# Performance work log

Measured on AMD Instinct MI355X. Metric: run time of the kernel, lower is better.

Reference implementation:

```python
import jax, jax.numpy as jnp
import numpy as np

B, T, C = 8, 1024, 1024   # batch, seq (== block_size), n_embed
H, D = 16, 64             # num_heads, head_size


def setup_inputs() -> dict:
    key = jax.random.key(0)
    kx, kq, kk, kv = jax.random.split(key, 4)
    scale = C ** -0.5  # mimic nn.Linear init scale roughly
    return {
        "x": jax.random.normal(kx, (B, T, C), dtype=jnp.float32),
        "Wq": jax.random.normal(kq, (H, C, D), dtype=jnp.float32) * scale,
        "Wk": jax.random.normal(kk, (H, C, D), dtype=jnp.float32) * scale,
        "Wv": jax.random.normal(kv, (H, C, D), dtype=jnp.float32) * scale,
    }


def reference(x, Wq, Wk, Wv):
    # Per-head Q/K/V projections (batched over heads instead of a Python loop)
    q = jnp.einsum("btc,hcd->bhtd", x, Wq)
    k = jnp.einsum("btc,hcd->bhtd", x, Wk)
    v = jnp.einsum("btc,hcd->bhtd", x, Wv)

    # scaled causal attention scores: [B, H, T, T]
    scores = jnp.einsum("bhtd,bhsd->bhts", q, k) * (D ** -0.5)
    causal = jnp.tril(jnp.ones((T, T), dtype=bool))
    scores = jnp.where(causal, scores, jnp.finfo(scores.dtype).min)
    attn = jax.nn.softmax(scores, axis=-1)

    out = jnp.einsum("bhts,bhsd->bhtd", attn, v)  # [B, H, T, D]
    # concat heads along last dim -> [B, T, H*D]
    return out.transpose(0, 2, 1, 3).reshape(B, T, H * D)
```

## Files before the change

### kernel.cpp

```cpp
#include <hip/hip_runtime.h>
#include <hip/hip_bf16.h>
#include <cstdint>


typedef __attribute__((ext_vector_type(8))) short short8;
typedef __attribute__((ext_vector_type(4))) short bfs4;
typedef __attribute__((ext_vector_type(4))) float f32x4;
typedef __attribute__((ext_vector_type(4))) int   i32x4;

__device__ __forceinline__ unsigned short f2bf(float f) {
  union { float f; unsigned int u; } v; v.f = f;
  unsigned int u = v.u;
  return (unsigned short)((u + 0x7fffu + ((u >> 16) & 1u)) >> 16);
}

__device__ __forceinline__ unsigned int pk_bf16(float a, float b) {
  union { __hip_bfloat162 h; unsigned int u; } cv;
  cv.h = __float22bfloat162_rn(make_float2(a, b));
  return cv.u;
}

__global__ __launch_bounds__(256) void k_convert_x(const float* __restrict__ x,
                                                   unsigned short* __restrict__ xb) {
  int g = blockIdx.x * 256 + threadIdx.x;
  const float4* xp = (const float4*)x + (size_t)g * 2;
  float4 a = xp[0], b = xp[1];
  short8 o;
  o[0] = (short)f2bf(a.x); o[1] = (short)f2bf(a.y);
  o[2] = (short)f2bf(a.z); o[3] = (short)f2bf(a.w);
  o[4] = (short)f2bf(b.x); o[5] = (short)f2bf(b.y);
  o[6] = (short)f2bf(b.z); o[7] = (short)f2bf(b.w);
  *(short8*)(xb + (size_t)g * 8) = o;
}

__global__ __launch_bounds__(256) void k_convert_w(const float* __restrict__ Wq,
                                                   const float* __restrict__ Wk,
                                                   const float* __restrict__ Wv,
                                                   unsigned short* __restrict__ Wt) {
  int g = blockIdx.x * 256 + threadIdx.x;
  int d  = g & 63;
  int cb = (g >> 6) & 127;
  int h  = (g >> 13) & 15;
  int p  = g >> 17;
  const float* W = (p == 0) ? Wq : (p == 1) ? Wk : Wv;
  const float* src = W + ((size_t)h * 1024 + cb * 8) * 64 + d;
  short8 o;
#pragma unroll
  for (int j = 0; j < 8; ++j) o[j] = (short)f2bf(src[(size_t)j * 64]);
  *(short8*)(Wt + (((size_t)p * 16 + h) * 64 + d) * 1024 + cb * 8) = o;
}

__global__ __launch_bounds__(256) void k_proj(const unsigned short* __restrict__ xb,
                                              const unsigned short* __restrict__ Wt,
                                              unsigned short* __restrict__ Qb,
                                              unsigned short* __restrict__ Kb,
                                              unsigned short* __restrict__ Vt) {
  __shared__ alignas(16) unsigned short As[8192];
  __shared__ alignas(16) unsigned short Bs[8192];
  const int p   = blockIdx.y;
  const int bx  = blockIdx.x;
  const int tid = threadIdx.x;
  const int lane = tid & 63, w = tid >> 6;
  const int ln = lane & 15, quad = lane >> 4;
  const int wm = w >> 1, wn = w & 1;

  const unsigned short* Abase;
  const unsigned short* Bbase;
  int m0, n0;
  const int c = bx & 7, j = bx >> 3;
  if (p < 2) {
    Abase = xb; Bbase = Wt + (size_t)p * 1048576;
    m0 = ((j >> 3) * 8 + c) * 128;
    n0 = (j & 7) * 128;
  } else {
    Abase = Wt + (size_t)2 * 1048576; Bbase = xb;
    n0 = ((j >> 3) * 8 + c) * 128;
    m0 = (j & 7) * 128;
  }

  i32x4 ra[4], rb[4];
  auto ld = [&](int kt) {
    const int c0 = kt * 64;
#pragma unroll
    for (int i = 0; i < 4; ++i) {
      int idx = i * 256 + tid;
      int iln = idx & 15, iq = (idx >> 4) & 3, imt = (idx >> 6) & 7, ikk = (idx >> 9) & 1;
      int row = imt * 16 + iln;
      int col = c0 + ikk * 32 + iq * 8;
      ra[i] = *(const i32x4*)(Abase + (size_t)(m0 + row) * 1024 + col);
      rb[i] = *(const i32x4*)(Bbase + (size_t)(n0 + row) * 1024 + col);
    }
  };

  f32x4 acc[4][4];
#pragma unroll
  for (int i = 0; i < 4; ++i)
#pragma unroll
    for (int jj = 0; jj < 4; ++jj) acc[i][jj] = (f32x4){0.f, 0.f, 0.f, 0.f};

  ld(0);
  for (int kt = 0; kt < 16; ++kt) {
#pragma unroll
    for (int i = 0; i < 4; ++i) {
      *(i32x4*)((char*)As + (size_t)(i * 256 + tid) * 16) = ra[i];
      *(i32x4*)((char*)Bs + (size_t)(i * 256 + tid) * 16) = rb[i];
    }
    __syncthreads();
    if (kt < 15) ld(kt + 1);

#pragma unroll
    for (int kk = 0; kk < 2; ++kk) {
      short8 af[4], bfr[4];
#pragma unroll
      for (int t4 = 0; t4 < 4; ++t4) {
        af[t4]  = *(const short8*)&As[(size_t)((((kk * 8 + wm * 4 + t4) * 4 + quad) * 16 + ln)) * 8];
        bfr[t4] = *(const short8*)&Bs[(size_t)((((kk * 8 + wn * 4 + t4) * 4 + quad) * 16 + ln)) * 8];
      }
#pragma unroll
      for (int mt = 0; mt < 4; ++mt)
#pragma unroll
        for (int nt = 0; nt < 4; ++nt)
          acc[mt][nt] = __builtin_amdgcn_mfma_f32_16x16x32_bf16(
              af[mt], bfr[nt], acc[mt][nt], 0, 0, 0);
    }
    __syncthreads();
  }

  unsigned short* outp = (p == 0) ? Qb : (p == 1) ? Kb : Vt;
#pragma unroll
  for (int mt = 0; mt < 4; ++mt)
#pragma unroll
    for (int nt = 0; nt < 4; ++nt)
#pragma unroll
      for (int r = 0; r < 4; ++r) {
        int m = m0 + (wm * 4 + mt) * 16 + quad * 4 + r;
        int n = n0 + (wn * 4 + nt) * 16 + ln;
        size_t addr;
        if (p < 2) {
          addr = ((size_t)(m >> 10) * 16 + (n >> 6)) * 65536 + (size_t)(m & 1023) * 64 + (n & 63);
        } else {
          addr = ((size_t)(n >> 10) * 1024 + m) * 1024 + (n & 1023);
        }
        outp[addr] = f2bf(acc[mt][nt][r]);
      }
}

__global__ __launch_bounds__(256) void k_attn(const unsigned short* __restrict__ Qb,
                                              const unsigned short* __restrict__ Kb,
                                              const unsigned short* __restrict__ Vt,
                                              float* __restrict__ out) {
  __shared__ alignas(16) unsigned short Ks[4096];
  __shared__ alignas(16) unsigned short Vs[4096];
  __shared__ alignas(16) unsigned short Ps[8192];
  const int bid = blockIdx.x;
  const int qb = 7 - (bid >> 7);
  const int bh = bid & 127;
  const int b = bh >> 4, h = bh & 15;
  const int tid = threadIdx.x, lane = tid & 63, w = tid >> 6;
  const int ln = lane & 15, quad = lane >> 4;

  i32x4 rk[2], rv[2];
  auto ldkv = [&](int kt) {
    const int s0 = kt * 64;
#pragma unroll
    for (int i = 0; i < 2; ++i) {
      int idx = i * 256 + tid;
      int iln = idx & 15, iq = (idx >> 4) & 3, ikk = (idx >> 6) & 1, it = (idx >> 7) & 3;
      rk[i] = *(const i32x4*)(Kb + ((size_t)bh * 1024 + s0 + it * 16 + iln) * 64 + ikk * 32 + iq * 8);
      rv[i] = *(const i32x4*)(Vt + ((size_t)bh * 64 + it * 16 + iln) * 1024 + s0 + ikk * 32 + iq * 8);
    }
  };

  short8 qf[2][2];
#pragma unroll
  for (int qt = 0; qt < 2; ++qt) {
    const int q = qb * 128 + qt * 64 + w * 16 + ln;
#pragma unroll
    for (int kk = 0; kk < 2; ++kk)
      qf[qt][kk] = *(const short8*)(Qb + ((size_t)bh * 1024 + q) * 64 + kk * 32 + quad * 8);
  }

  f32x4 o[2][4];
#pragma unroll
  for (int qt = 0; qt < 2; ++qt)
#pragma unroll
    for (int dt = 0; dt < 4; ++dt) o[qt][dt] = (f32x4){0.f, 0.f, 0.f, 0.f};
  float l_i[2] = {0.f, 0.f};
  const float sc = 0.18033688011112042f;
  const float FM = 16.0f;

  const int ktmax = 2 * qb + 1;
  ldkv(0);

  for (int kt = 0; kt <= ktmax; ++kt) {
    const int s0 = kt * 64;
#pragma unroll
    for (int i = 0; i < 2; ++i) {
      *(i32x4*)((char*)Ks + (size_t)(i * 256 + tid) * 16) = rk[i];
      *(i32x4*)((char*)Vs + (size_t)(i * 256 + tid) * 16) = rv[i];
    }
    __syncthreads();
    if (kt < ktmax) ldkv(kt + 1);

    f32x4 st[2][4];
#pragma unroll
    for (int s = 0; s < 4; ++s) {
      st[0][s] = (f32x4){0.f, 0.f, 0.f, 0.f};
      st[1][s] = (f32x4){0.f, 0.f, 0.f, 0.f};
#pragma unroll
      for (int kk = 0; kk < 2; ++kk) {
        short8 kf = *(const short8*)&Ks[(size_t)(((s * 2 + kk) * 4 + quad) * 16 + ln) * 8];
        st[0][s] = __builtin_amdgcn_mfma_f32_16x16x32_bf16(kf, qf[0][kk], st[0][s], 0, 0, 0);
        st[1][s] = __builtin_amdgcn_mfma_f32_16x16x32_bf16(kf, qf[1][kk], st[1][s], 0, 0, 0);
      }
    }

#pragma unroll
    for (int qt = 0; qt < 2; ++qt) {
      const int q = qb * 128 + qt * 64 + w * 16 + ln;
      const bool masked = (kt >= 2 * qb + qt);
      float pv[4][4];
      float rs = 0.f;
#pragma unroll
      for (int s = 0; s < 4; ++s)
#pragma unroll
        for (int r = 0; r < 4; ++r) {
          float v = fmaf(st[qt][s][r], sc, -FM);
          if (masked) {
            int sidx = s0 + s * 16 + quad * 4 + r;
            if (sidx > q) v = -1.0e30f;
          }
          float e = __builtin_amdgcn_exp2f(v);
          pv[s][r] = e;
          rs += e;
        }
      rs += __shfl_xor(rs, 16);
      rs += __shfl_xor(rs, 32);
      l_i[qt] += rs;

      unsigned short* Pq = Ps + (w * 2 + qt) * 1024;
#pragma unroll
      for (int s = 0; s < 4; ++s) {
        union { bfs4 v; unsigned int u[2]; } pk;
        pk.u[0] = pk_bf16(pv[s][0], pv[s][1]);
        pk.u[1] = pk_bf16(pv[s][2], pv[s][3]);
        *(bfs4*)&Pq[(s * 2 + (quad >> 1)) * 128 + ln * 8 + (quad & 1) * 4] = pk.v;
      }
    }

#pragma unroll
    for (int kk = 0; kk < 2; ++kk) {
      short8 pf0 = *(const short8*)&Ps[(size_t)(w * 2 + 0) * 1024 + (size_t)((kk * 4 + quad) * 16 + ln) * 8];
      short8 pf1 = *(const short8*)&Ps[(size_t)(w * 2 + 1) * 1024 + (size_t)((kk * 4 + quad) * 16 + ln) * 8];
#pragma unroll
      for (int dt = 0; dt < 4; ++dt) {
        short8 vf = *(const short8*)&Vs[(size_t)(((dt * 2 + kk) * 4 + quad) * 16 + ln) * 8];
        o[0][dt] = __builtin_amdgcn_mfma_f32_16x16x32_bf16(vf, pf0, o[0][dt], 0, 0, 0);
        o[1][dt] = __builtin_amdgcn_mfma_f32_16x16x32_bf16(vf, pf1, o[1][dt], 0, 0, 0);
      }
    }

    __syncthreads();
  }

#pragma unroll
  for (int qt = 0; qt < 2; ++qt) {
    const int q = qb * 128 + qt * 64 + w * 16 + ln;
    const float rl = 1.0f / l_i[qt];
#pragma unroll
    for (int dt = 0; dt < 4; ++dt) {
      float4 ov;
      ov.x = o[qt][dt][0] * rl; ov.y = o[qt][dt][1] * rl;
      ov.z = o[qt][dt][2] * rl; ov.w = o[qt][dt][3] * rl;
      *(float4*)(out + ((size_t)b * 1024 + q) * 1024 + h * 64 + dt * 16 + quad * 4) = ov;
    }
  }
}

extern "C" void kernel_launch(void* const* d_in, const int* in_sizes, int n_in,
                              void* d_out, int out_size, void* d_ws, size_t ws_size,
                              hipStream_t stream) {
  const float* x  = (const float*)d_in[0];
  const float* Wq = (const float*)d_in[1];
  const float* Wk = (const float*)d_in[2];
  const float* Wv = (const float*)d_in[3];
  float* out = (float*)d_out;

  unsigned short* ws = (unsigned short*)d_ws;
  unsigned short* xb = ws;
  unsigned short* Wt = ws + 8388608;
  unsigned short* Qb = ws + 11534336;
  unsigned short* Kb = ws + 19922944;
  unsigned short* Vt = ws + 28311552;

  hipLaunchKernelGGL(k_convert_x, dim3(4096), dim3(256), 0, stream, x, xb);
  hipLaunchKernelGGL(k_convert_w, dim3(1536), dim3(256), 0, stream, Wq, Wk, Wv, Wt);
  hipLaunchKernelGGL(k_proj, dim3(512, 3), dim3(256), 0, stream, xb, Wt, Qb, Kb, Vt);
  hipLaunchKernelGGL(k_attn, dim3(1024), dim3(256), 0, stream, Qb, Kb, Vt, out);
}
```

Baseline: 232.0 us.

## Load GEMM and attention tiles directly into LDS via global_load_lds

Replaces the register-staged prefetch (global load to VGPRs, then LDS store) in both the projection GEMM and the attention kernel with direct global-to-LDS 16-byte loads. This cuts VGPR pressure and the LDS write instructions. It also drops the software prefetch of the next tile, so each iteration now waits on its own load before computing, and global latency is no longer overlapped with the MFMA work. No waitcnt is added beyond __syncthreads, so correctness relies on the compiler inserting vmcnt waits.

```diff
diff --git a/kernel.cpp b/kernel.cpp
--- a/kernel.cpp
+++ b/kernel.cpp
@@ -6,7 +6,6 @@
 typedef __attribute__((ext_vector_type(8))) short short8;
 typedef __attribute__((ext_vector_type(4))) short bfs4;
 typedef __attribute__((ext_vector_type(4))) float f32x4;
-typedef __attribute__((ext_vector_type(4))) int   i32x4;
 
 __device__ __forceinline__ unsigned short f2bf(float f) {
   union { float f; unsigned int u; } v; v.f = f;
@@ -18,6 +17,12 @@
   union { __hip_bfloat162 h; unsigned int u; } cv;
   cv.h = __float22bfloat162_rn(make_float2(a, b));
   return cv.u;
+}
+
+__device__ __forceinline__ void gload_lds16(const void* g, void* l) {
+  __builtin_amdgcn_global_load_lds(
+      (const __attribute__((address_space(1))) void*)g,
+      (__attribute__((address_space(3))) void*)l, 16, 0, 0);
 }
 
 __global__ __launch_bounds__(256) void k_convert_x(const float* __restrict__ x,
@@ -78,8 +83,7 @@
     m0 = (j & 7) * 128;
   }
 
-  i32x4 ra[4], rb[4];
-  auto ld = [&](int kt) {
+  auto stage = [&](int kt) {
     const int c0 = kt * 64;
 #pragma unroll
     for (int i = 0; i < 4; ++i) {
@@ -87,8 +91,9 @@
       int iln = idx & 15, iq = (idx >> 4) & 3, imt = (idx >> 6) & 7, ikk = (idx >> 9) & 1;
       int row = imt * 16 + iln;
       int col = c0 + ikk * 32 + iq * 8;
-      ra[i] = *(const i32x4*)(Abase + (size_t)(m0 + row) * 1024 + col);
-      rb[i] = *(const i32x4*)(Bbase + (size_t)(n0 + row) * 1024 + col);
+      const int chunk0 = i * 256 + (tid & 192);
+      gload_lds16(Abase + (size_t)(m0 + row) * 1024 + col, (char*)As + (size_t)chunk0 * 16);
+      gload_lds16(Bbase + (size_t)(n0 + row) * 1024 + col, (char*)Bs + (size_t)chunk0 * 16);
     }
   };
 
@@ -98,15 +103,9 @@
 #pragma unroll
     for (int jj = 0; jj < 4; ++jj) acc[i][jj] = (f32x4){0.f, 0.f, 0.f, 0.f};
 
-  ld(0);
   for (int kt = 0; kt < 16; ++kt) {
-#pragma unroll
-    for (int i = 0; i < 4; ++i) {
-      *(i32x4*)((char*)As + (size_t)(i * 256 + tid) * 16) = ra[i];
-      *(i32x4*)((char*)Bs + (size_t)(i * 256 + tid) * 16) = rb[i];
-    }
-    __syncthreads();
-    if (kt < 15) ld(kt + 1);
+    stage(kt);
+    __syncthreads();
 
 #pragma unroll
     for (int kk = 0; kk < 2; ++kk) {
@@ -159,18 +158,6 @@
   const int tid = threadIdx.x, lane = tid & 63, w = tid >> 6;
   const int ln = lane & 15, quad = lane >> 4;
 
-  i32x4 rk[2], rv[2];
-  auto ldkv = [&](int kt) {
-    const int s0 = kt * 64;
-#pragma unroll
-    for (int i = 0; i < 2; ++i) {
-      int idx = i * 256 + tid;
-      int iln = idx & 15, iq = (idx >> 4) & 3, ikk = (idx >> 6) & 1, it = (idx >> 7) & 3;
-      rk[i] = *(const i32x4*)(Kb + ((size_t)bh * 1024 + s0 + it * 16 + iln) * 64 + ikk * 32 + iq * 8);
-      rv[i] = *(const i32x4*)(Vt + ((size_t)bh * 64 + it * 16 + iln) * 1024 + s0 + ikk * 32 + iq * 8);
-    }
-  };
-
   short8 qf[2][2];
 #pragma unroll
   for (int qt = 0; qt < 2; ++qt) {
@@ -190,17 +177,20 @@
   const float FM = 16.0f;
 
   const int ktmax = 2 * qb + 1;
-  ldkv(0);
 
   for (int kt = 0; kt <= ktmax; ++kt) {
     const int s0 = kt * 64;
 #pragma unroll
     for (int i = 0; i < 2; ++i) {
-      *(i32x4*)((char*)Ks + (size_t)(i * 256 + tid) * 16) = rk[i];
-      *(i32x4*)((char*)Vs + (size_t)(i * 256 + tid) * 16) = rv[i];
-    }
-    __syncthreads();
-    if (kt < ktmax) ldkv(kt + 1);
+      int idx = i * 256 + tid;
+      int iln = idx & 15, iq = (idx >> 4) & 3, ikk = (idx >> 6) & 1, it = (idx >> 7) & 3;
+      const int chunk0 = i * 256 + (tid & 192);
+      gload_lds16(Kb + ((size_t)bh * 1024 + s0 + it * 16 + iln) * 64 + ikk * 32 + iq * 8,
+                  (char*)Ks + (size_t)chunk0 * 16);
+      gload_lds16(Vt + ((size_t)bh * 64 + it * 16 + iln) * 1024 + s0 + ikk * 32 + iq * 8,
+                  (char*)Vs + (size_t)chunk0 * 16);
+    }
+    __syncthreads();
 
     f32x4 st[2][4];
 #pragma unroll
```

New measurement: 237.4 us. +2.3%, slower.

## Rewrite projection GEMM with 256x256 tiles and double-buffered direct-to-LDS loads

Applied to the files above, without the earlier changes.

The QKV projection GEMM moves from 128x128 tiles with 256 threads to 256x256 tiles with 512 threads (8 waves), which raises operand reuse per block. Global loads now go straight into double-buffered LDS via global_load_lds, so the register staging round-trip disappears. Loads for the next k-step are interleaved with the MFMA phases using barriers and setprio. In exchange, 384 large blocks at one block per CU may underfill the GPU and leave a tail, and LDS use is much higher.

```diff
diff --git a/kernel.cpp b/kernel.cpp
--- a/kernel.cpp
+++ b/kernel.cpp
@@ -18,6 +18,12 @@
   union { __hip_bfloat162 h; unsigned int u; } cv;
   cv.h = __float22bfloat162_rn(make_float2(a, b));
   return cv.u;
+}
+
+__device__ __forceinline__ void gload_lds16(const void* g, void* l) {
+  __builtin_amdgcn_global_load_lds(
+      (const __attribute__((address_space(1))) void*)g,
+      (__attribute__((address_space(3))) void*)l, 16, 0, 0);
 }
 
 __global__ __launch_bounds__(256) void k_convert_x(const float* __restrict__ x,
@@ -50,91 +56,133 @@
   *(short8*)(Wt + (((size_t)p * 16 + h) * 64 + d) * 1024 + cb * 8) = o;
 }
 
-__global__ __launch_bounds__(256) void k_proj(const unsigned short* __restrict__ xb,
-                                              const unsigned short* __restrict__ Wt,
-                                              unsigned short* __restrict__ Qb,
-                                              unsigned short* __restrict__ Kb,
-                                              unsigned short* __restrict__ Vt) {
-  __shared__ alignas(16) unsigned short As[8192];
-  __shared__ alignas(16) unsigned short Bs[8192];
+__global__ __launch_bounds__(512, 1) void k_proj(const unsigned short* __restrict__ xb,
+                                                 const unsigned short* __restrict__ Wt,
+                                                 unsigned short* __restrict__ Qb,
+                                                 unsigned short* __restrict__ Kb,
+                                                 unsigned short* __restrict__ Vt) {
+  __shared__ alignas(16) unsigned short As[2][2][8192];
+  __shared__ alignas(16) unsigned short Bs[2][2][8192];
   const int p   = blockIdx.y;
   const int bx  = blockIdx.x;
   const int tid = threadIdx.x;
   const int lane = tid & 63, w = tid >> 6;
   const int ln = lane & 15, quad = lane >> 4;
-  const int wm = w >> 1, wn = w & 1;
+  const int wm = w >> 2, wn = w & 3;
 
   const unsigned short* Abase;
   const unsigned short* Bbase;
   int m0, n0;
-  const int c = bx & 7, j = bx >> 3;
   if (p < 2) {
     Abase = xb; Bbase = Wt + (size_t)p * 1048576;
-    m0 = ((j >> 3) * 8 + c) * 128;
-    n0 = (j & 7) * 128;
+    m0 = (bx >> 2) * 256;
+    n0 = (bx & 3) * 256;
   } else {
     Abase = Wt + (size_t)2 * 1048576; Bbase = xb;
-    n0 = ((j >> 3) * 8 + c) * 128;
-    m0 = (j & 7) * 128;
-  }
-
-  i32x4 ra[4], rb[4];
-  auto ld = [&](int kt) {
-    const int c0 = kt * 64;
-#pragma unroll
-    for (int i = 0; i < 4; ++i) {
-      int idx = i * 256 + tid;
-      int iln = idx & 15, iq = (idx >> 4) & 3, imt = (idx >> 6) & 7, ikk = (idx >> 9) & 1;
-      int row = imt * 16 + iln;
-      int col = c0 + ikk * 32 + iq * 8;
-      ra[i] = *(const i32x4*)(Abase + (size_t)(m0 + row) * 1024 + col);
-      rb[i] = *(const i32x4*)(Bbase + (size_t)(n0 + row) * 1024 + col);
+    m0 = (bx & 3) * 256;
+    n0 = (bx >> 2) * 256;
+  }
+
+  auto stageA = [&](int buf, int half, int t) {
+#pragma unroll
+    for (int i = 0; i < 2; ++i) {
+      int c = i * 512 + tid;
+      int iln = c & 15, iq = (c >> 4) & 3, lm = (c >> 6) & 7, ikk = (c >> 9) & 1;
+      int row = m0 + half * 128 + lm * 16 + iln;
+      int col = t * 64 + ikk * 32 + iq * 8;
+      const int chunk0 = i * 512 + w * 64;
+      gload_lds16(Abase + (size_t)row * 1024 + col,
+                  (char*)&As[buf][half][0] + (size_t)chunk0 * 16);
     }
   };
-
-  f32x4 acc[4][4];
-#pragma unroll
-  for (int i = 0; i < 4; ++i)
+  auto stageB = [&](int buf, int half, int t) {
+#pragma unroll
+    for (int i = 0; i < 2; ++i) {
+      int c = i * 512 + tid;
+      int iln = c & 15, iq = (c >> 4) & 3, lm = (c >> 6) & 7, ikk = (c >> 9) & 1;
+      int row = n0 + half * 128 + lm * 16 + iln;
+      int col = t * 64 + ikk * 32 + iq * 8;
+      const int chunk0 = i * 512 + w * 64;
+      gload_lds16(Bbase + (size_t)row * 1024 + col,
+                  (char*)&Bs[buf][half][0] + (size_t)chunk0 * 16);
+    }
+  };
+
+  f32x4 acc[8][4];
+#pragma unroll
+  for (int i = 0; i < 8; ++i)
 #pragma unroll
     for (int jj = 0; jj < 4; ++jj) acc[i][jj] = (f32x4){0.f, 0.f, 0.f, 0.f};
 
-  ld(0);
-  for (int kt = 0; kt < 16; ++kt) {
-#pragma unroll
-    for (int i = 0; i < 4; ++i) {
-      *(i32x4*)((char*)As + (size_t)(i * 256 + tid) * 16) = ra[i];
-      *(i32x4*)((char*)Bs + (size_t)(i * 256 + tid) * 16) = rb[i];
-    }
-    __syncthreads();
-    if (kt < 15) ld(kt + 1);
-
-#pragma unroll
-    for (int kk = 0; kk < 2; ++kk) {
-      short8 af[4], bfr[4];
-#pragma unroll
-      for (int t4 = 0; t4 < 4; ++t4) {
-        af[t4]  = *(const short8*)&As[(size_t)((((kk * 8 + wm * 4 + t4) * 4 + quad) * 16 + ln)) * 8];
-        bfr[t4] = *(const short8*)&Bs[(size_t)((((kk * 8 + wn * 4 + t4) * 4 + quad) * 16 + ln)) * 8];
-      }
-#pragma unroll
-      for (int mt = 0; mt < 4; ++mt)
-#pragma unroll
-        for (int nt = 0; nt < 4; ++nt)
-          acc[mt][nt] = __builtin_amdgcn_mfma_f32_16x16x32_bf16(
-              af[mt], bfr[nt], acc[mt][nt], 0, 0, 0);
-    }
-    __syncthreads();
+  stageA(0, 0, 0); stageA(0, 1, 0); stageB(0, 0, 0); stageB(0, 1, 0);
+  asm volatile("s_waitcnt vmcnt(0)" ::: "memory");
+  __builtin_amdgcn_s_barrier();
+
+  for (int it = 0; it < 8; ++it) {
+    const int t1 = 2 * it + 1;
+    const int t2 = 2 * it + 2;
+    const bool st2 = (t2 < 16);
+#pragma unroll
+    for (int ph = 0; ph < 8; ++ph) {
+      const int rbuf = ph >> 2;
+      const int q = ph & 3;
+      const int mh = q >> 1, nq = q & 1;
+
+      const unsigned short* Ah = As[rbuf][wm];
+      const unsigned short* Bh = Bs[rbuf][wn >> 1];
+      short8 af[4][2], bf[2][2];
+#pragma unroll
+      for (int m = 0; m < 4; ++m)
+#pragma unroll
+        for (int kk = 0; kk < 2; ++kk)
+          af[m][kk] = *(const short8*)&Ah[(size_t)(kk * 512 + (mh * 4 + m) * 64 + quad * 16 + ln) * 8];
+#pragma unroll
+      for (int n = 0; n < 2; ++n)
+#pragma unroll
+        for (int kk = 0; kk < 2; ++kk)
+          bf[n][kk] = *(const short8*)&Bh[(size_t)(kk * 512 + ((wn & 1) * 4 + nq * 2 + n) * 64 + quad * 16 + ln) * 8];
+
+      if (rbuf == 0) {
+        if      (q == 0) stageA(1, 0, t1);
+        else if (q == 1) stageA(1, 1, t1);
+        else if (q == 2) stageB(1, 0, t1);
+        else             stageB(1, 1, t1);
+      } else if (st2) {
+        if      (q == 0) stageA(0, 0, t2);
+        else if (q == 1) stageA(0, 1, t2);
+        else if (q == 2) stageB(0, 0, t2);
+        else             stageB(0, 1, t2);
+      }
+
+      __builtin_amdgcn_sched_barrier(0);
+      __builtin_amdgcn_s_barrier();
+      __builtin_amdgcn_sched_barrier(0);
+
+      __builtin_amdgcn_s_setprio(1);
+#pragma unroll
+      for (int m = 0; m < 4; ++m)
+#pragma unroll
+        for (int n = 0; n < 2; ++n)
+#pragma unroll
+          for (int kk = 0; kk < 2; ++kk)
+            acc[mh * 4 + m][nq * 2 + n] = __builtin_amdgcn_mfma_f32_16x16x32_bf16(
+                af[m][kk], bf[n][kk], acc[mh * 4 + m][nq * 2 + n], 0, 0, 0);
+      __builtin_amdgcn_s_setprio(0);
+
+      if (q == 3) asm volatile("s_waitcnt vmcnt(0)" ::: "memory");
+      __builtin_amdgcn_s_barrier();
+    }
   }
 
   unsigned short* outp = (p == 0) ? Qb : (p == 1) ? Kb : Vt;
 #pragma unroll
-  for (int mt = 0; mt < 4; ++mt)
+  for (int mt = 0; mt < 8; ++mt)
 #pragma unroll
     for (int nt = 0; nt < 4; ++nt)
 #pragma unroll
       for (int r = 0; r < 4; ++r) {
-        int m = m0 + (wm * 4 + mt) * 16 + quad * 4 + r;
-        int n = n0 + (wn * 4 + nt) * 16 + ln;
+        int m = m0 + wm * 128 + mt * 16 + quad * 4 + r;
+        int n = n0 + wn * 64 + nt * 16 + ln;
         size_t addr;
         if (p < 2) {
           addr = ((size_t)(m >> 10) * 16 + (n >> 6)) * 65536 + (size_t)(m & 1023) * 64 + (n & 63);
@@ -295,6 +343,6 @@
 
   hipLaunchKernelGGL(k_convert_x, dim3(4096), dim3(256), 0, stream, x, xb);
   hipLaunchKernelGGL(k_convert_w, dim3(1536), dim3(256), 0, stream, Wq, Wk, Wv, Wt);
-  hipLaunchKernelGGL(k_proj, dim3(512, 3), dim3(256), 0, stream, xb, Wt, Qb, Kb, Vt);
+  hipLaunchKernelGGL(k_proj, dim3(128, 3), dim3(512), 0, stream, xb, Wt, Qb, Kb, Vt);
   hipLaunchKernelGGL(k_attn, dim3(1024), dim3(256), 0, stream, Qb, Kb, Vt, out);
 }
```

Result: no change. 230.3 us (-0.7%).

## Rewrite projection GEMM with direct global-to-LDS triple-buffered pipeline and larger tiles

Applied to the files above, without the earlier changes.

The QKV projection GEMM now loads tiles straight from global memory into LDS with global_load_lds, skipping the register round trip. It uses a three-stage LDS ring with vmcnt-based waits, so one barrier per k-step replaces two. Tiles grow to 256x128 with a k-step of 32, so each wave issues 32 MFMAs per step, and the grid halves to 256x3 blocks. Costs are higher register pressure (launch bounds now request 2 blocks per CU) and a changed block-to-tile mapping that drops the previous L2 swizzle.

```diff
diff --git a/kernel.cpp b/kernel.cpp
--- a/kernel.cpp
+++ b/kernel.cpp
@@ -18,6 +18,12 @@
   union { __hip_bfloat162 h; unsigned int u; } cv;
   cv.h = __float22bfloat162_rn(make_float2(a, b));
   return cv.u;
+}
+
+__device__ __forceinline__ void gload_lds16(const void* g, void* l) {
+  __builtin_amdgcn_global_load_lds(
+      (const __attribute__((address_space(1))) void*)g,
+      (__attribute__((address_space(3))) void*)l, 16, 0, 0);
 }
 
 __global__ __launch_bounds__(256) void k_convert_x(const float* __restrict__ x,
@@ -50,13 +56,13 @@
   *(short8*)(Wt + (((size_t)p * 16 + h) * 64 + d) * 1024 + cb * 8) = o;
 }
 
-__global__ __launch_bounds__(256) void k_proj(const unsigned short* __restrict__ xb,
-                                              const unsigned short* __restrict__ Wt,
-                                              unsigned short* __restrict__ Qb,
-                                              unsigned short* __restrict__ Kb,
-                                              unsigned short* __restrict__ Vt) {
-  __shared__ alignas(16) unsigned short As[8192];
-  __shared__ alignas(16) unsigned short Bs[8192];
+__global__ __launch_bounds__(256, 2) void k_proj(const unsigned short* __restrict__ xb,
+                                                 const unsigned short* __restrict__ Wt,
+                                                 unsigned short* __restrict__ Qb,
+                                                 unsigned short* __restrict__ Kb,
+                                                 unsigned short* __restrict__ Vt) {
+  __shared__ alignas(16) unsigned short As[3][8192];
+  __shared__ alignas(16) unsigned short Bs[3][4096];
   const int p   = blockIdx.y;
   const int bx  = blockIdx.x;
   const int tid = threadIdx.x;
@@ -67,74 +73,84 @@
   const unsigned short* Abase;
   const unsigned short* Bbase;
   int m0, n0;
-  const int c = bx & 7, j = bx >> 3;
   if (p < 2) {
     Abase = xb; Bbase = Wt + (size_t)p * 1048576;
-    m0 = ((j >> 3) * 8 + c) * 128;
-    n0 = (j & 7) * 128;
+    m0 = (bx >> 3) * 256;
+    n0 = (bx & 7) * 128;
   } else {
     Abase = Wt + (size_t)2 * 1048576; Bbase = xb;
-    n0 = ((j >> 3) * 8 + c) * 128;
-    m0 = (j & 7) * 128;
-  }
-
-  i32x4 ra[4], rb[4];
-  auto ld = [&](int kt) {
-    const int c0 = kt * 64;
-#pragma unroll
-    for (int i = 0; i < 4; ++i) {
-      int idx = i * 256 + tid;
-      int iln = idx & 15, iq = (idx >> 4) & 3, imt = (idx >> 6) & 7, ikk = (idx >> 9) & 1;
-      int row = imt * 16 + iln;
-      int col = c0 + ikk * 32 + iq * 8;
-      ra[i] = *(const i32x4*)(Abase + (size_t)(m0 + row) * 1024 + col);
-      rb[i] = *(const i32x4*)(Bbase + (size_t)(n0 + row) * 1024 + col);
+    m0 = (bx & 3) * 256;
+    n0 = (bx >> 2) * 128;
+  }
+
+  auto stage = [&](int t, int buf) {
+    const int c0 = t * 32;
+#pragma unroll
+    for (int j = 0; j < 4; ++j) {
+      int cch = j * 256 + tid;
+      int iln = cch & 15, iq = (cch >> 4) & 3, mb = cch >> 6;
+      gload_lds16(Abase + (size_t)(m0 + mb * 16 + iln) * 1024 + c0 + iq * 8,
+                  (char*)&As[buf][0] + (size_t)(j * 256 + w * 64) * 16);
+    }
+#pragma unroll
+    for (int j = 0; j < 2; ++j) {
+      int cch = j * 256 + tid;
+      int iln = cch & 15, iq = (cch >> 4) & 3, nb = cch >> 6;
+      gload_lds16(Bbase + (size_t)(n0 + nb * 16 + iln) * 1024 + c0 + iq * 8,
+                  (char*)&Bs[buf][0] + (size_t)(j * 256 + w * 64) * 16);
     }
   };
 
-  f32x4 acc[4][4];
-#pragma unroll
-  for (int i = 0; i < 4; ++i)
+  f32x4 acc[8][4];
+#pragma unroll
+  for (int i = 0; i < 8; ++i)
 #pragma unroll
     for (int jj = 0; jj < 4; ++jj) acc[i][jj] = (f32x4){0.f, 0.f, 0.f, 0.f};
 
-  ld(0);
-  for (int kt = 0; kt < 16; ++kt) {
-#pragma unroll
-    for (int i = 0; i < 4; ++i) {
-      *(i32x4*)((char*)As + (size_t)(i * 256 + tid) * 16) = ra[i];
-      *(i32x4*)((char*)Bs + (size_t)(i * 256 + tid) * 16) = rb[i];
-    }
-    __syncthreads();
-    if (kt < 15) ld(kt + 1);
-
-#pragma unroll
-    for (int kk = 0; kk < 2; ++kk) {
-      short8 af[4], bfr[4];
-#pragma unroll
-      for (int t4 = 0; t4 < 4; ++t4) {
-        af[t4]  = *(const short8*)&As[(size_t)((((kk * 8 + wm * 4 + t4) * 4 + quad) * 16 + ln)) * 8];
-        bfr[t4] = *(const short8*)&Bs[(size_t)((((kk * 8 + wn * 4 + t4) * 4 + quad) * 16 + ln)) * 8];
-      }
-#pragma unroll
-      for (int mt = 0; mt < 4; ++mt)
-#pragma unroll
-        for (int nt = 0; nt < 4; ++nt)
-          acc[mt][nt] = __builtin_amdgcn_mfma_f32_16x16x32_bf16(
-              af[mt], bfr[nt], acc[mt][nt], 0, 0, 0);
-    }
-    __syncthreads();
+  stage(0, 0);
+  stage(1, 1);
+  asm volatile("s_waitcnt vmcnt(6)" ::: "memory");
+  __builtin_amdgcn_s_barrier();
+
+  int rb = 0;
+  for (int t = 0; t < 32; ++t) {
+    short8 af[8], bfv[4];
+#pragma unroll
+    for (int m = 0; m < 8; ++m)
+      af[m] = *(const short8*)&As[rb][(size_t)((wm * 8 + m) * 64 + quad * 16 + ln) * 8];
+#pragma unroll
+    for (int n = 0; n < 4; ++n)
+      bfv[n] = *(const short8*)&Bs[rb][(size_t)((wn * 4 + n) * 64 + quad * 16 + ln) * 8];
+
+    int sb = rb + 2; if (sb >= 3) sb -= 3;
+    if (t <= 29) stage(t + 2, sb);
+
+#pragma unroll
+    for (int m = 0; m < 8; ++m)
+#pragma unroll
+      for (int n = 0; n < 4; ++n)
+        acc[m][n] = __builtin_amdgcn_mfma_f32_16x16x32_bf16(
+            af[m], bfv[n], acc[m][n], 0, 0, 0);
+
+    if (t < 30) {
+      asm volatile("s_waitcnt vmcnt(6)" ::: "memory");
+      __builtin_amdgcn_s_barrier();
+    } else if (t == 30) {
+      asm volatile("s_waitcnt vmcnt(0)" ::: "memory");
+      __builtin_amdgcn_s_barrier();
+    }
+    if (++rb == 3) rb = 0;
   }
 
   unsigned short* outp = (p == 0) ? Qb : (p == 1) ? Kb : Vt;
 #pragma unroll
-  for (int mt = 0; mt < 4; ++mt)
+  for (int mt = 0; mt < 8; ++mt)
 #pragma unroll
     for (int nt = 0; nt < 4; ++nt)
 #pragma unroll
       for (int r = 0; r < 4; ++r) {
-        int m = m0 + (wm * 4 + mt) * 16 + quad * 4 + r;
-        int n = n0 + (wn * 4 + nt) * 16 + ln;
+        int m = m0 + wm * 128 + mt * 16 + quad * 4 + r;
+        int n = n0 + wn * 64 + nt * 16 + ln;
         size_t addr;
         if (p < 2) {
           addr = ((size_t)(m >> 10) * 16 + (n >> 6)) * 65536 + (size_t)(m & 1023) * 64 + (n & 63);
@@ -295,6 +311,6 @@
 
   hipLaunchKernelGGL(k_convert_x, dim3(4096), dim3(256), 0, stream, x, xb);
   hipLaunchKernelGGL(k_convert_w, dim3(1536), dim3(256), 0, stream, Wq, Wk, Wv, Wt);
-  hipLaunchKernelGGL(k_proj, dim3(512, 3), dim3(256), 0, stream, xb, Wt, Qb, Kb, Vt);
+  hipLaunchKernelGGL(k_proj, dim3(256, 3), dim3(256), 0, stream, xb, Wt, Qb, Kb, Vt);
   hipLaunchKernelGGL(k_attn, dim3(1024), dim3(256), 0, stream, Qb, Kb, Vt, out);
 }
```

Measured after the change: 213.0 us (median of 2 runs). 1.09x faster.
